# Kernel tuning notes

Hardware: AMD Instinct MI355X
Metric: run time of the kernel (lower is better)

## Reference

```python
import jax, jax.numpy as jnp
import numpy as np

B, T, E, C, H = 8, 96, 96, 256, 8
D = C // H
HID = int(C * 4.0)
EPS = 1e-5


def _ln(x, g, b):
    m = x.mean(-1, keepdims=True)
    v = ((x - m) ** 2).mean(-1, keepdims=True)
    return (x - m) * jax.lax.rsqrt(v + EPS) * g + b


def setup_inputs() -> dict:
    key = jax.random.key(0)
    ks = jax.random.split(key, 20)
    s = 0.02
    inp = {
        "x": jax.random.normal(ks[0], (B, T, E, C), jnp.float32),
        "adj_mask": jax.random.uniform(ks[1], (E, E), jnp.float32) * 2.0 - 1.0,  # direction cosines in [-1,1]
        "n1_g": jnp.ones((C,)), "n1_b": jnp.zeros((C,)),
        "s_wq": jax.random.normal(ks[2], (C, C)) * s,
        "s_wk": jax.random.normal(ks[3], (C, C)) * s,
        "s_wv": jax.random.normal(ks[4], (C, C)) * s,
        "s_wp": jax.random.normal(ks[5], (C, C)) * s,
        "s_bp": jnp.zeros((C,)),
        "s_ng": jnp.ones((C,)), "s_nb": jnp.zeros((C,)),
        "s_gamma": jax.random.normal(ks[6], (1,)) * 0.1,
        "n2_g": jnp.ones((C,)), "n2_b": jnp.zeros((C,)),
        "t_wq": jax.random.normal(ks[7], (C, C)) * s,
        "t_wk": jax.random.normal(ks[8], (C, C)) * s,
        "t_wv": jax.random.normal(ks[9], (C, C)) * s,
        "t_wp": jax.random.normal(ks[10], (C, C)) * s,
        "t_bp": jnp.zeros((C,)),
        "t_gamma": jax.random.normal(ks[11], (1,)) * 0.1,
        "n3_g": jnp.ones((C,)), "n3_b": jnp.zeros((C,)),
        "m_w1": jax.random.normal(ks[12], (C, HID)) * s,
        "m_b1": jnp.zeros((HID,)),
        "m_w2": jax.random.normal(ks[13], (HID, C)) * s,
        "m_b2": jnp.zeros((C,)),
    }
    return inp


def _interp_linear_T(x, t_new):
    # x: [B, T, E, C]; torch F.interpolate(mode='linear', align_corners=False) over T
    t = x.shape[1]
    scale = t / t_new
    src = (jnp.arange(t_new, dtype=jnp.float32) + 0.5) * scale - 0.5
    src = jnp.clip(src, 0.0, t - 1)
    i0 = jnp.floor(src).astype(jnp.int32)
    i1 = jnp.minimum(i0 + 1, t - 1)
    w = (src - i0.astype(jnp.float32))[None, :, None, None]
    return x[:, i0] * (1.0 - w) + x[:, i1] * w


def reference(x, adj_mask, n1_g, n1_b, s_wq, s_wk, s_wv, s_wp, s_bp, s_ng, s_nb, s_gamma,
              n2_g, n2_b, t_wq, t_wk, t_wv, t_wp, t_bp, t_gamma,
              n3_g, n3_b, m_w1, m_b1, m_w2, m_b2):
    b, t, e, c = x.shape
    h, d = H, C // H

    # ---- spatial geometric-cosine attention (per frame) ----
    xs = _ln(x, n1_g, n1_b)                                    # identity inside spatial_attn
    q = (xs @ s_wq).reshape(b, t, e, h, d)
    k = (xs @ s_wk).reshape(b, t, e, h, d)
    v = (xs @ s_wv).reshape(b, t, e, h, d)
    attn = jnp.einsum('btqhd,btkhd->bthqk', q, k)
    attn = (attn * adj_mask + 1.0) * 0.5                        # masked-cosine, no softmax
    o = jnp.einsum('bthqk,btkhd->btqhd', attn, v).reshape(b, t, e, c)
    o = _ln(o @ s_wp + s_bp, s_ng, s_nb)
    x = x + (xs + s_gamma * o)

    # ---- temporal softmax attention (per edge) ----
    xt = _ln(x, n2_g, n2_b)
    q = (xt @ t_wq).reshape(b, t, e, h, d)
    k = (xt @ t_wk).reshape(b, t, e, h, d)
    v = (xt @ t_wv).reshape(b, t, e, h, d)
    attn = jnp.einsum('bqehd,bkehd->behqk', q, k) * (d ** -0.5)
    attn = jax.nn.softmax(attn, axis=-1)
    o = jnp.einsum('behqk,bkehd->bqehd', attn, v).reshape(b, t, e, c)
    o = o @ t_wp + t_bp
    x = x + t_gamma * o

    # ---- MLP ----
    xm = _ln(x, n3_g, n3_b)
    x = x + (jax.nn.gelu(xm @ m_w1 + m_b1, approximate=False) @ m_w2 + m_b2)

    # ---- temporal downsampling (interpolate) ----
    t_new = t // 2 + t % 2
    if t > 1:
        x = _interp_linear_T(x, t_new)
    return x
```

## Files before the change

### kernel.cpp

```cpp
#include <hip/hip_runtime.h>
#include <cmath>

constexpr int BB = 8, TT = 96, EE = 96, CC = 256, HHD = 8, DDm = 32;
constexpr int NTOK = BB * TT * EE;
constexpr int TOUT = TT / 2;

typedef unsigned short u16;
typedef short bf16x8 __attribute__((ext_vector_type(8)));
typedef float f32x4 __attribute__((ext_vector_type(4)));

__device__ __forceinline__ float bf2f(u16 u) {
  union { unsigned int i; float f; } v; v.i = ((unsigned int)u) << 16; return v.f;
}
__device__ __forceinline__ u16 f2bf(float f) {
  union { unsigned int i; float f; } v; v.f = f;
  return (u16)((v.i + 0x7FFFu + ((v.i >> 16) & 1u)) >> 16);
}
__device__ __forceinline__ float wsum(float v) {
#pragma unroll
  for (int off = 32; off; off >>= 1) v += __shfl_xor(v, off);
  return v;
}
__device__ __forceinline__ float gelu_f(float x) {
  return 0.5f * x * (1.0f + erff(x * 0.70710678118654752f));
}
__device__ __forceinline__ int remap_row(int row, int mode) {
  if (mode == 0) return row;
  int b = row / (TT * EE);
  int rem = row - b * (TT * EE);
  if (mode == 1) { int t = rem / EE, e = rem - t * EE; return (b * EE + e) * TT + t; }
  int e = rem / TT, t = rem - e * TT;
  return (b * TT + t) * EE + e;
}

struct WPtr8 { const float* p[8]; };
__global__ void k_transpose8(WPtr8 src, u16* __restrict__ dst) {
  const float* in = src.p[blockIdx.y];
  u16* out = dst + (size_t)blockIdx.y * 65536;
  int idx = blockIdx.x * 256 + threadIdx.x;
  int k = idx >> 8, c = idx & 255;
  out[c * 256 + k] = f2bf(in[idx]);
}

__global__ void k_transpose(const float* __restrict__ in, u16* __restrict__ out, int K, int Nc, int n) {
  int idx = blockIdx.x * 256 + threadIdx.x;
  if (idx < n) {
    int k = idx / Nc, c = idx - k * Nc;
    out[c * K + k] = f2bf(in[idx]);
  }
}

__global__ void k_cvt(const float* __restrict__ in, u16* __restrict__ out, int n) {
  int idx = blockIdx.x * 256 + threadIdx.x;
  if (idx < n) out[idx] = f2bf(in[idx]);
}

__global__ __launch_bounds__(256) void k_ln_in(const float* __restrict__ x,
                                               u16* __restrict__ A, const float* __restrict__ g,
                                               const float* __restrict__ b) {
  int wv = threadIdx.x >> 6, lane = threadIdx.x & 63;
  long tok = (long)blockIdx.x * 4 + wv;
  int c = lane * 4;
  long off = tok * CC + c;
  float4 v = *(const float4*)(x + off);
  float s = v.x + v.y + v.z + v.w;
  float sq = v.x * v.x + v.y * v.y + v.z * v.z + v.w * v.w;
  s = wsum(s); sq = wsum(sq);
  float m = s * (1.0f / CC);
  float rs = rsqrtf(sq * (1.0f / CC) - m * m + 1e-5f);
  float4 gv = *(const float4*)(g + c);
  float4 bv = *(const float4*)(b + c);
  ushort4 o;
  o.x = f2bf((v.x - m) * rs * gv.x + bv.x);
  o.y = f2bf((v.y - m) * rs * gv.y + bv.y);
  o.z = f2bf((v.z - m) * rs * gv.z + bv.z);
  o.w = f2bf((v.w - m) * rs * gv.w + bv.w);
  *(ushort4*)(A + off) = o;
}

__global__ __launch_bounds__(256) void k_ln_f32(const float* __restrict__ X, u16* __restrict__ A,
                                                const float* __restrict__ g, const float* __restrict__ b) {
  int wv = threadIdx.x >> 6, lane = threadIdx.x & 63;
  long tok = (long)blockIdx.x * 4 + wv;
  int c = lane * 4;
  long off = tok * CC + c;
  float4 v = *(const float4*)(X + off);
  float s = v.x + v.y + v.z + v.w;
  float sq = v.x * v.x + v.y * v.y + v.z * v.z + v.w * v.w;
  s = wsum(s); sq = wsum(sq);
  float m = s * (1.0f / CC);
  float rs = rsqrtf(sq * (1.0f / CC) - m * m + 1e-5f);
  float4 gv = *(const float4*)(g + c);
  float4 bv = *(const float4*)(b + c);
  ushort4 o;
  o.x = f2bf((v.x - m) * rs * gv.x + bv.x);
  o.y = f2bf((v.y - m) * rs * gv.y + bv.y);
  o.z = f2bf((v.z - m) * rs * gv.z + bv.z);
  o.w = f2bf((v.w - m) * rs * gv.w + bv.w);
  *(ushort4*)(A + off) = o;
}

__global__ __launch_bounds__(256) void k_sp_combine(const float* __restrict__ xin, float* __restrict__ X,
                                                    u16* __restrict__ A, const u16* __restrict__ P,
                                                    const float* __restrict__ n1g, const float* __restrict__ n1b,
                                                    const float* __restrict__ sg,
                                                    const float* __restrict__ s_ng, const float* __restrict__ s_nb,
                                                    const float* __restrict__ n2g, const float* __restrict__ n2b) {
  int wv = threadIdx.x >> 6, lane = threadIdx.x & 63;
  long tok = (long)blockIdx.x * 4 + wv;
  int c = lane * 4;
  long off = tok * CC + c;
  float4 xv = *(const float4*)(xin + off);
  float s1 = xv.x + xv.y + xv.z + xv.w;
  float q1 = xv.x * xv.x + xv.y * xv.y + xv.z * xv.z + xv.w * xv.w;
  s1 = wsum(s1); q1 = wsum(q1);
  float m1 = s1 * (1.0f / CC);
  float r1 = rsqrtf(q1 * (1.0f / CC) - m1 * m1 + 1e-5f);
  float4 g1 = *(const float4*)(n1g + c);
  float4 b1 = *(const float4*)(n1b + c);
  float xs0 = (xv.x - m1) * r1 * g1.x + b1.x;
  float xs1 = (xv.y - m1) * r1 * g1.y + b1.y;
  float xs2 = (xv.z - m1) * r1 * g1.z + b1.z;
  float xs3 = (xv.w - m1) * r1 * g1.w + b1.w;
  ushort4 up = *(const ushort4*)(P + off);
  float4 p = make_float4(bf2f(up.x), bf2f(up.y), bf2f(up.z), bf2f(up.w));
  float s = p.x + p.y + p.z + p.w;
  float sq = p.x * p.x + p.y * p.y + p.z * p.z + p.w * p.w;
  s = wsum(s); sq = wsum(sq);
  float m = s * (1.0f / CC);
  float rs = rsqrtf(sq * (1.0f / CC) - m * m + 1e-5f);
  float4 ug = *(const float4*)(s_ng + c);
  float4 ub = *(const float4*)(s_nb + c);
  float o0 = (p.x - m) * rs * ug.x + ub.x;
  float o1 = (p.y - m) * rs * ug.y + ub.y;
  float o2 = (p.z - m) * rs * ug.z + ub.z;
  float o3 = (p.w - m) * rs * ug.w + ub.w;
  float gsg = sg[0];
  float x0 = xv.x + xs0 + gsg * o0;
  float x1 = xv.y + xs1 + gsg * o1;
  float x2 = xv.z + xs2 + gsg * o2;
  float x3 = xv.w + xs3 + gsg * o3;
  *(float4*)(X + off) = make_float4(x0, x1, x2, x3);
  float s2 = x0 + x1 + x2 + x3;
  float sq2 = x0 * x0 + x1 * x1 + x2 * x2 + x3 * x3;
  s2 = wsum(s2); sq2 = wsum(sq2);
  float m2 = s2 * (1.0f / CC);
  float rs2 = rsqrtf(sq2 * (1.0f / CC) - m2 * m2 + 1e-5f);
  float4 g2 = *(const float4*)(n2g + c);
  float4 b2 = *(const float4*)(n2b + c);
  ushort4 o;
  o.x = f2bf((x0 - m2) * rs2 * g2.x + b2.x);
  o.y = f2bf((x1 - m2) * rs2 * g2.y + b2.y);
  o.z = f2bf((x2 - m2) * rs2 * g2.z + b2.z);
  o.w = f2bf((x3 - m2) * rs2 * g2.w + b2.w);
  *(ushort4*)(A + off) = o;
}

__global__ __launch_bounds__(256) void k_gemm128(const u16* __restrict__ act, const u16* __restrict__ Wt,
                                                 const float* __restrict__ bias, const float* __restrict__ gptr,
                                                 u16* __restrict__ outB, float* __restrict__ Xacc,
                                                 int Kd, int Nc, int lda, int ldb, int epi, int remap) {
  __shared__ __align__(16) u16 smem[128 * 136];
  u16* As = smem;
  u16* Bs = smem + 4096;
  int m0 = blockIdx.y * 128, n0 = blockIdx.x * 128;
  int tid = threadIdx.x;
  int wv = tid >> 6, lane = tid & 63, lm = lane & 15, quad = lane >> 4;
  int wr = wv >> 1, wc = wv & 1;
  f32x4 acc[4][4];
#pragma unroll
  for (int i = 0; i < 4; i++)
#pragma unroll
    for (int j = 0; j < 4; j++) acc[i][j] = (f32x4){0.f, 0.f, 0.f, 0.f};

  for (int kk = 0; kk < Kd; kk += 32) {
#pragma unroll
    for (int j = 0; j < 2; j++) {
      int cid = j * 256 + wv * 64 + lane;
      int row = cid >> 2, seg = cid & 3;
      const u16* ga = act + (long)(m0 + row) * lda + kk + seg * 8;
      const u16* gb = Wt + (long)(n0 + row) * ldb + kk + seg * 8;
      u16* la = &As[(j * 256 + wv * 64) * 8];
      u16* lb = &Bs[(j * 256 + wv * 64) * 8];
      __builtin_amdgcn_global_load_lds(ga, la, 16, 0, 0);
      __builtin_amdgcn_global_load_lds(gb, lb, 16, 0, 0);
    }
    __syncthreads();
    bf16x8 af[4], bfv[4];
#pragma unroll
    for (int t = 0; t < 4; t++) {
      af[t] = *(const bf16x8*)&As[(wr * 64 + t * 16 + lm) * 32 + quad * 8];
      bfv[t] = *(const bf16x8*)&Bs[(wc * 64 + t * 16 + lm) * 32 + quad * 8];
    }
#pragma unroll
    for (int ti = 0; ti < 4; ti++)
#pragma unroll
      for (int tj = 0; tj < 4; tj++)
        acc[ti][tj] = __builtin_amdgcn_mfma_f32_16x16x32_bf16(af[ti], bfv[tj], acc[ti][tj], 0, 0, 0);
    __syncthreads();
  }

  if (epi == 3) {
    float gm = gptr ? gptr[0] : 1.0f;
#pragma unroll
    for (int tj = 0; tj < 4; tj++) {
      int col = n0 + wc * 64 + tj * 16 + lm;
      float bv = bias ? bias[col] : 0.0f;
#pragma unroll
      for (int ti = 0; ti < 4; ti++)
#pragma unroll
        for (int r = 0; r < 4; r++) {
          int row = remap_row(m0 + wr * 64 + ti * 16 + quad * 4 + r, remap);
          Xacc[(long)row * Nc + col] += gm * (acc[ti][tj][r] + bv);
        }
    }
  } else {
#pragma unroll
    for (int tj = 0; tj < 4; tj++) {
      int col = wc * 64 + tj * 16 + lm;
      float bv = (epi >= 1 && bias) ? bias[n0 + col] : 0.0f;
#pragma unroll
      for (int ti = 0; ti < 4; ti++)
#pragma unroll
        for (int r = 0; r < 4; r++) {
          float vv = acc[ti][tj][r] + bv;
          if (epi == 2) vv = gelu_f(vv);
          smem[(wr * 64 + ti * 16 + quad * 4 + r) * 136 + col] = f2bf(vv);
        }
    }
    __syncthreads();
#pragma unroll
    for (int p = 0; p < 8; p++) {
      int idx = p * 256 + tid;
      int row = idx >> 4, c8 = idx & 15;
      int grow = remap_row(m0 + row, remap);
      *(uint4*)(outB + (long)grow * Nc + n0 + c8 * 8) = *(const uint4*)&smem[row * 136 + c8 * 8];
    }
  }
}

__global__ __launch_bounds__(384) void k_sp_attn(const u16* __restrict__ QKV, const u16* __restrict__ adj,
                                                 u16* __restrict__ O) {
  __shared__ __align__(16) u16 Qs[96 * 32];
  __shared__ __align__(16) u16 Ks[96 * 32];
  __shared__ __align__(16) u16 Vs[96 * 32];
  __shared__ __align__(16) u16 Ss[96 * 96];
  int blk = blockIdx.x;
  int h = blk & 7, t = (blk >> 3) % TT, b = blk / (8 * TT);
  long base = ((long)(b * TT + t) * EE) * 768 + h * DDm;
  int tid = threadIdx.x;
  {
    int row = tid >> 2, seg = tid & 3;
    long goff = base + (long)row * 768 + seg * 8;
    *(uint4*)&Qs[row * 32 + seg * 8] = *(const uint4*)(QKV + goff);
    *(uint4*)&Ks[row * 32 + seg * 8] = *(const uint4*)(QKV + goff + 256);
    *(uint4*)&Vs[row * 32 + seg * 8] = *(const uint4*)(QKV + goff + 512);
#pragma unroll
    for (int i = 0; i < 3; i++) {
      int off = tid * 24 + i * 8;
      *(uint4*)&Ss[off] = *(const uint4*)(adj + off);
    }
  }
  __syncthreads();
  int wv = tid >> 6, lane = tid & 63, lm = lane & 15, quad = lane >> 4;
  bf16x8 aq = *(const bf16x8*)&Qs[(wv * 16 + lm) * 32 + quad * 8];
  f32x4 sc[6];
#pragma unroll
  for (int j = 0; j < 6; j++) {
    bf16x8 bk = *(const bf16x8*)&Ks[(j * 16 + lm) * 32 + quad * 8];
    f32x4 z = (f32x4){0.f, 0.f, 0.f, 0.f};
    sc[j] = __builtin_amdgcn_mfma_f32_16x16x32_bf16(aq, bk, z, 0, 0, 0);
  }
  u16 sv[6][4];
#pragma unroll
  for (int j = 0; j < 6; j++) {
    int col = j * 16 + lm;
#pragma unroll
    for (int r = 0; r < 4; r++) {
      int row = wv * 16 + quad * 4 + r;
      float a = bf2f(Ss[row * 96 + col]);
      sv[j][r] = f2bf((sc[j][r] * a + 1.0f) * 0.5f);
    }
  }
  __syncthreads();
#pragma unroll
  for (int j = 0; j < 6; j++) {
    int col = j * 16 + lm;
#pragma unroll
    for (int r = 0; r < 4; r++) Ss[(wv * 16 + quad * 4 + r) * 96 + col] = sv[j][r];
  }
  __syncthreads();
  f32x4 oc[2];
  oc[0] = (f32x4){0.f, 0.f, 0.f, 0.f};
  oc[1] = (f32x4){0.f, 0.f, 0.f, 0.f};
#pragma unroll
  for (int ks = 0; ks < 3; ks++) {
    bf16x8 as = *(const bf16x8*)&Ss[(wv * 16 + lm) * 96 + ks * 32 + quad * 8];
#pragma unroll
    for (int n = 0; n < 2; n++) {
      bf16x8 bv;
#pragma unroll
      for (int jj = 0; jj < 8; jj++)
        bv[jj] = (short)Vs[(ks * 32 + quad * 8 + jj) * 32 + n * 16 + lm];
      oc[n] = __builtin_amdgcn_mfma_f32_16x16x32_bf16(as, bv, oc[n], 0, 0, 0);
    }
  }
  long obase = ((long)(b * TT + t) * EE) * CC + h * DDm;
#pragma unroll
  for (int n = 0; n < 2; n++)
#pragma unroll
    for (int r = 0; r < 4; r++) {
      int row = wv * 16 + quad * 4 + r;
      O[obase + (long)row * CC + n * 16 + lm] = f2bf(oc[n][r]);
    }
}

__global__ __launch_bounds__(384) void k_tp_attn(const u16* __restrict__ QKV, u16* __restrict__ O) {
  __shared__ __align__(16) u16 Qs[96 * 32];
  __shared__ __align__(16) u16 Ks[96 * 32];
  __shared__ __align__(16) u16 Vs[96 * 32];
  __shared__ __align__(16) u16 Ss[96 * 96];
  int blk = blockIdx.x;
  int h = blk & 7, e = (blk >> 3) % EE, b = blk / (8 * EE);
  long base = ((long)(b * EE + e) * TT) * 768 + h * DDm;
  int tid = threadIdx.x;
  {
    int row = tid >> 2, seg = tid & 3;
    long goff = base + (long)row * 768 + seg * 8;
    *(uint4*)&Qs[row * 32 + seg * 8] = *(const uint4*)(QKV + goff);
    *(uint4*)&Ks[row * 32 + seg * 8] = *(const uint4*)(QKV + goff + 256);
    *(uint4*)&Vs[row * 32 + seg * 8] = *(const uint4*)(QKV + goff + 512);
  }
  __syncthreads();
  int wv = tid >> 6, lane = tid & 63, lm = lane & 15, quad = lane >> 4;
  bf16x8 aq = *(const bf16x8*)&Qs[(wv * 16 + lm) * 32 + quad * 8];
  f32x4 sc[6];
#pragma unroll
  for (int j = 0; j < 6; j++) {
    bf16x8 bk = *(const bf16x8*)&Ks[(j * 16 + lm) * 32 + quad * 8];
    f32x4 z = (f32x4){0.f, 0.f, 0.f, 0.f};
    sc[j] = __builtin_amdgcn_mfma_f32_16x16x32_bf16(aq, bk, z, 0, 0, 0);
  }
  const float scale = 0.17677669529663687f;
#pragma unroll
  for (int r = 0; r < 4; r++) {
    float mx = -1e30f;
#pragma unroll
    for (int j = 0; j < 6; j++) { sc[j][r] *= scale; mx = fmaxf(mx, sc[j][r]); }
#pragma unroll
    for (int mask = 1; mask < 16; mask <<= 1) mx = fmaxf(mx, __shfl_xor(mx, mask));
    float sum = 0.f;
#pragma unroll
    for (int j = 0; j < 6; j++) { float p = __expf(sc[j][r] - mx); sc[j][r] = p; sum += p; }
#pragma unroll
    for (int mask = 1; mask < 16; mask <<= 1) sum += __shfl_xor(sum, mask);
    float inv = 1.0f / sum;
#pragma unroll
    for (int j = 0; j < 6; j++) sc[j][r] *= inv;
  }
#pragma unroll
  for (int j = 0; j < 6; j++) {
    int col = j * 16 + lm;
#pragma unroll
    for (int r = 0; r < 4; r++) Ss[(wv * 16 + quad * 4 + r) * 96 + col] = f2bf(sc[j][r]);
  }
  __syncthreads();
  f32x4 oc[2];
  oc[0] = (f32x4){0.f, 0.f, 0.f, 0.f};
  oc[1] = (f32x4){0.f, 0.f, 0.f, 0.f};
#pragma unroll
  for (int ks = 0; ks < 3; ks++) {
    bf16x8 as = *(const bf16x8*)&Ss[(wv * 16 + lm) * 96 + ks * 32 + quad * 8];
#pragma unroll
    for (int n = 0; n < 2; n++) {
      bf16x8 bv;
#pragma unroll
      for (int jj = 0; jj < 8; jj++)
        bv[jj] = (short)Vs[(ks * 32 + quad * 8 + jj) * 32 + n * 16 + lm];
      oc[n] = __builtin_amdgcn_mfma_f32_16x16x32_bf16(as, bv, oc[n], 0, 0, 0);
    }
  }
  long obase = ((long)(b * EE + e) * TT) * CC + h * DDm;
#pragma unroll
  for (int n = 0; n < 2; n++)
#pragma unroll
    for (int r = 0; r < 4; r++) {
      int row = wv * 16 + quad * 4 + r;
      O[obase + (long)row * CC + n * 16 + lm] = f2bf(oc[n][r]);
    }
}

__global__ __launch_bounds__(256) void k_down(const float* __restrict__ X, float* __restrict__ out) {
  long i4 = ((long)blockIdx.x * 256 + threadIdx.x) * 4;
  long tmp = i4;
  int c = (int)(tmp & 255); tmp >>= 8;
  int e = (int)(tmp % EE); tmp /= EE;
  int i = (int)(tmp % TOUT);
  int b = (int)(tmp / TOUT);
  long src0 = (((long)b * TT + 2 * i) * EE + e) * CC + c;
  float4 a = *(const float4*)(X + src0);
  float4 bb = *(const float4*)(X + src0 + (long)EE * CC);
  float4 o = make_float4(0.5f * (a.x + bb.x), 0.5f * (a.y + bb.y),
                         0.5f * (a.z + bb.z), 0.5f * (a.w + bb.w));
  *(float4*)(out + i4) = o;
}

extern "C" void kernel_launch(void* const* d_in, const int* in_sizes, int n_in,
                              void* d_out, int out_size, void* d_ws, size_t ws_size,
                              hipStream_t stream) {
  (void)in_sizes; (void)n_in; (void)out_size; (void)ws_size;
  const float* x   = (const float*)d_in[0];
  const float* adj = (const float*)d_in[1];
  const float* n1g = (const float*)d_in[2];
  const float* n1b = (const float*)d_in[3];
  const float* swq = (const float*)d_in[4];
  const float* swk = (const float*)d_in[5];
  const float* swv = (const float*)d_in[6];
  const float* swp = (const float*)d_in[7];
  const float* sbp = (const float*)d_in[8];
  const float* sng = (const float*)d_in[9];
  const float* snb = (const float*)d_in[10];
  const float* sg  = (const float*)d_in[11];
  const float* n2g = (const float*)d_in[12];
  const float* n2b = (const float*)d_in[13];
  const float* twq = (const float*)d_in[14];
  const float* twk = (const float*)d_in[15];
  const float* twv = (const float*)d_in[16];
  const float* twp = (const float*)d_in[17];
  const float* tbp = (const float*)d_in[18];
  const float* tg  = (const float*)d_in[19];
  const float* n3g = (const float*)d_in[20];
  const float* n3b = (const float*)d_in[21];
  const float* mw1 = (const float*)d_in[22];
  const float* mb1 = (const float*)d_in[23];
  const float* mw2 = (const float*)d_in[24];
  const float* mb2 = (const float*)d_in[25];
  float* out = (float*)d_out;

  size_t nc = (size_t)NTOK * CC;
  float* X  = (float*)d_ws;
  u16* A    = (u16*)(X + nc);
  u16* QKV  = A + nc;
  u16* Pb   = QKV;
  u16* Hh   = QKV;
  u16* wts  = QKV + 3 * nc;
  u16* swq_t = wts;
  u16* swp_t = wts + 3 * 65536;
  u16* twq_t = wts + 4 * 65536;
  u16* twp_t = wts + 7 * 65536;
  u16* w1_t  = wts + 8 * 65536;
  u16* w2_t  = w1_t + 262144;
  u16* adj_b = w2_t + 262144;

  WPtr8 w8; w8.p[0] = swq; w8.p[1] = swk; w8.p[2] = swv; w8.p[3] = swp;
  w8.p[4] = twq; w8.p[5] = twk; w8.p[6] = twv; w8.p[7] = twp;
  k_transpose8<<<dim3(256, 8), 256, 0, stream>>>(w8, wts);
  k_transpose<<<(256 * 1024 + 255) / 256, 256, 0, stream>>>(mw1, w1_t, 256, 1024, 256 * 1024);
  k_transpose<<<(1024 * 256 + 255) / 256, 256, 0, stream>>>(mw2, w2_t, 1024, 256, 1024 * 256);
  k_cvt<<<(EE * EE + 255) / 256, 256, 0, stream>>>(adj, adj_b, EE * EE);

  auto gemm = [&](const u16* act, const u16* Wt, const float* bias, const float* gamma,
                  u16* outB, float* Xacc, int Kd, int Nc, int lda, int ldb, int epi, int remap, int M) {
    dim3 g(Nc / 128, M / 128);
    k_gemm128<<<g, 256, 0, stream>>>(act, Wt, bias, gamma, outB, Xacc, Kd, Nc, lda, ldb, epi, remap);
  };

  int lnBlocks = NTOK / 4;

  k_ln_in<<<lnBlocks, 256, 0, stream>>>(x, A, n1g, n1b);
  gemm(A, swq_t, nullptr, nullptr, QKV, nullptr, 256, 768, 256, 256, 0, 0, NTOK);
  k_sp_attn<<<BB * TT * HHD, 384, 0, stream>>>(QKV, adj_b, A);
  gemm(A, swp_t, sbp, nullptr, Pb, nullptr, 256, 256, 256, 256, 1, 0, NTOK);
  k_sp_combine<<<lnBlocks, 256, 0, stream>>>(x, X, A, Pb, n1g, n1b, sg, sng, snb, n2g, n2b);

  gemm(A, twq_t, nullptr, nullptr, QKV, nullptr, 256, 768, 256, 256, 0, 1, NTOK);
  k_tp_attn<<<BB * EE * HHD, 384, 0, stream>>>(QKV, A);
  gemm(A, twp_t, tbp, tg, nullptr, X, 256, 256, 256, 256, 3, 2, NTOK);

  k_ln_f32<<<lnBlocks, 256, 0, stream>>>(X, A, n3g, n3b);
  for (int hf = 0; hf < 2; hf++) {
    long r0 = (long)hf * (NTOK / 2);
    gemm(A + r0 * CC, w1_t, mb1, nullptr, Hh, nullptr, 256, 1024, 256, 256, 2, 0, NTOK / 2);
    gemm(Hh, w2_t, mb2, nullptr, nullptr, X + r0 * CC, 1024, 256, 1024, 1024, 3, 0, NTOK / 2);
  }

  long outElems = (long)BB * TOUT * EE * CC;
  k_down<<<(int)(outElems / 4 / 256), 256, 0, stream>>>(X, out);
}
```

Before: 809.3 us.

## Switch to edge-major layout after spatial stage, fuse downsample into MLP GEMM, double-buffer loads

```diff
diff --git a/kernel.cpp b/kernel.cpp
--- a/kernel.cpp
+++ b/kernel.cpp
@@ -23,14 +23,6 @@
 }
 __device__ __forceinline__ float gelu_f(float x) {
   return 0.5f * x * (1.0f + erff(x * 0.70710678118654752f));
-}
-__device__ __forceinline__ int remap_row(int row, int mode) {
-  if (mode == 0) return row;
-  int b = row / (TT * EE);
-  int rem = row - b * (TT * EE);
-  if (mode == 1) { int t = rem / EE, e = rem - t * EE; return (b * EE + e) * TT + t; }
-  int e = rem / TT, t = rem - e * TT;
-  return (b * TT + t) * EE + e;
 }
 
 struct WPtr8 { const float* p[8]; };
@@ -110,6 +102,10 @@
   long tok = (long)blockIdx.x * 4 + wv;
   int c = lane * 4;
   long off = tok * CC + c;
+  int b = (int)(tok / (TT * EE));
+  int rem = (int)(tok - (long)b * TT * EE);
+  int t = rem / EE, e = rem - t * EE;
+  long offB = ((long)(b * EE + e) * TT + t) * CC + c;
   float4 xv = *(const float4*)(xin + off);
   float s1 = xv.x + xv.y + xv.z + xv.w;
   float q1 = xv.x * xv.x + xv.y * xv.y + xv.z * xv.z + xv.w * xv.w;
@@ -140,7 +136,7 @@
   float x1 = xv.y + xs1 + gsg * o1;
   float x2 = xv.z + xs2 + gsg * o2;
   float x3 = xv.w + xs3 + gsg * o3;
-  *(float4*)(X + off) = make_float4(x0, x1, x2, x3);
+  *(float4*)(X + offB) = make_float4(x0, x1, x2, x3);
   float s2 = x0 + x1 + x2 + x3;
   float sq2 = x0 * x0 + x1 * x1 + x2 * x2 + x3 * x3;
   s2 = wsum(s2); sq2 = wsum(sq2);
@@ -153,16 +149,15 @@
   o.y = f2bf((x1 - m2) * rs2 * g2.y + b2.y);
   o.z = f2bf((x2 - m2) * rs2 * g2.z + b2.z);
   o.w = f2bf((x3 - m2) * rs2 * g2.w + b2.w);
-  *(ushort4*)(A + off) = o;
+  *(ushort4*)(A + offB) = o;
 }
 
 __global__ __launch_bounds__(256) void k_gemm128(const u16* __restrict__ act, const u16* __restrict__ Wt,
                                                  const float* __restrict__ bias, const float* __restrict__ gptr,
                                                  u16* __restrict__ outB, float* __restrict__ Xacc,
-                                                 int Kd, int Nc, int lda, int ldb, int epi, int remap) {
-  __shared__ __align__(16) u16 smem[128 * 136];
-  u16* As = smem;
-  u16* Bs = smem + 4096;
+                                                 float* __restrict__ outF,
+                                                 int Kd, int Nc, int lda, int ldb, int epi, int hbase) {
+  __shared__ __align__(16) u16 smem[16384];
   int m0 = blockIdx.y * 128, n0 = blockIdx.x * 128;
   int tid = threadIdx.x;
   int wv = tid >> 6, lane = tid & 63, lm = lane & 15, quad = lane >> 4;
@@ -173,19 +168,28 @@
 #pragma unroll
     for (int j = 0; j < 4; j++) acc[i][j] = (f32x4){0.f, 0.f, 0.f, 0.f};
 
-  for (int kk = 0; kk < Kd; kk += 32) {
+  auto stage = [&](int kt, int buf) {
+    u16* As = smem + buf * 4096;
+    u16* Bs = smem + 8192 + buf * 4096;
 #pragma unroll
     for (int j = 0; j < 2; j++) {
       int cid = j * 256 + wv * 64 + lane;
       int row = cid >> 2, seg = cid & 3;
-      const u16* ga = act + (long)(m0 + row) * lda + kk + seg * 8;
-      const u16* gb = Wt + (long)(n0 + row) * ldb + kk + seg * 8;
-      u16* la = &As[(j * 256 + wv * 64) * 8];
-      u16* lb = &Bs[(j * 256 + wv * 64) * 8];
-      __builtin_amdgcn_global_load_lds(ga, la, 16, 0, 0);
-      __builtin_amdgcn_global_load_lds(gb, lb, 16, 0, 0);
-    }
-    __syncthreads();
+      const u16* ga = act + (long)(m0 + row) * lda + kt * 32 + seg * 8;
+      const u16* gb = Wt + (long)(n0 + row) * ldb + kt * 32 + seg * 8;
+      __builtin_amdgcn_global_load_lds(ga, &As[(j * 256 + wv * 64) * 8], 16, 0, 0);
+      __builtin_amdgcn_global_load_lds(gb, &Bs[(j * 256 + wv * 64) * 8], 16, 0, 0);
+    }
+  };
+
+  int nk = Kd / 32;
+  stage(0, 0);
+  __syncthreads();
+  for (int kt = 0; kt < nk; kt++) {
+    int cur = kt & 1;
+    if (kt + 1 < nk) stage(kt + 1, cur ^ 1);
+    const u16* As = smem + cur * 4096;
+    const u16* Bs = smem + 8192 + cur * 4096;
     bf16x8 af[4], bfv[4];
 #pragma unroll
     for (int t = 0; t < 4; t++) {
@@ -210,31 +214,59 @@
       for (int ti = 0; ti < 4; ti++)
 #pragma unroll
         for (int r = 0; r < 4; r++) {
-          int row = remap_row(m0 + wr * 64 + ti * 16 + quad * 4 + r, remap);
+          int row = m0 + wr * 64 + ti * 16 + quad * 4 + r;
           Xacc[(long)row * Nc + col] += gm * (acc[ti][tj][r] + bv);
         }
     }
+  } else if (epi == 4) {
+#pragma unroll
+    for (int tj = 0; tj < 4; tj++) {
+      int col = n0 + wc * 64 + tj * 16 + lm;
+      float bv = bias ? bias[col] : 0.0f;
+#pragma unroll
+      for (int ti = 0; ti < 4; ti++) {
+        int lr0 = wr * 64 + ti * 16 + quad * 4;
+#pragma unroll
+        for (int pr = 0; pr < 2; pr++) {
+          int lr = lr0 + pr * 2;
+          float v0 = Xacc[(long)(m0 + lr) * Nc + col] + acc[ti][tj][pr * 2] + bv;
+          float v1 = Xacc[(long)(m0 + lr + 1) * Nc + col] + acc[ti][tj][pr * 2 + 1] + bv;
+          int gr = hbase + m0 + lr;
+          int b = gr / (EE * TT);
+          int rem = gr - b * (EE * TT);
+          int e = rem / TT, t = rem - e * TT;
+          long orow = (long)(b * TOUT + (t >> 1)) * EE + e;
+          outF[orow * CC + col] = 0.5f * (v0 + v1);
+        }
+      }
+    }
   } else {
 #pragma unroll
-    for (int tj = 0; tj < 4; tj++) {
-      int col = wc * 64 + tj * 16 + lm;
-      float bv = (epi >= 1 && bias) ? bias[n0 + col] : 0.0f;
-#pragma unroll
-      for (int ti = 0; ti < 4; ti++)
-#pragma unroll
-        for (int r = 0; r < 4; r++) {
-          float vv = acc[ti][tj][r] + bv;
-          if (epi == 2) vv = gelu_f(vv);
-          smem[(wr * 64 + ti * 16 + quad * 4 + r) * 136 + col] = f2bf(vv);
+    for (int h = 0; h < 2; h++) {
+      if (wr == h) {
+#pragma unroll
+        for (int tj = 0; tj < 4; tj++) {
+          int col = wc * 64 + tj * 16 + lm;
+          float bv = (epi >= 1 && bias) ? bias[n0 + col] : 0.0f;
+#pragma unroll
+          for (int ti = 0; ti < 4; ti++)
+#pragma unroll
+            for (int r = 0; r < 4; r++) {
+              float vv = acc[ti][tj][r] + bv;
+              if (epi == 2) vv = gelu_f(vv);
+              smem[(ti * 16 + quad * 4 + r) * 136 + col] = f2bf(vv);
+            }
         }
-    }
-    __syncthreads();
-#pragma unroll
-    for (int p = 0; p < 8; p++) {
-      int idx = p * 256 + tid;
-      int row = idx >> 4, c8 = idx & 15;
-      int grow = remap_row(m0 + row, remap);
-      *(uint4*)(outB + (long)grow * Nc + n0 + c8 * 8) = *(const uint4*)&smem[row * 136 + c8 * 8];
+      }
+      __syncthreads();
+#pragma unroll
+      for (int p = 0; p < 4; p++) {
+        int idx = p * 256 + tid;
+        int row = idx >> 4, c8 = idx & 15;
+        *(uint4*)(outB + (long)(m0 + h * 64 + row) * Nc + n0 + c8 * 8) =
+            *(const uint4*)&smem[row * 136 + c8 * 8];
+      }
+      __syncthreads();
     }
   }
 }
@@ -388,21 +420,6 @@
       int row = wv * 16 + quad * 4 + r;
       O[obase + (long)row * CC + n * 16 + lm] = f2bf(oc[n][r]);
     }
-}
-
-__global__ __launch_bounds__(256) void k_down(const float* __restrict__ X, float* __restrict__ out) {
-  long i4 = ((long)blockIdx.x * 256 + threadIdx.x) * 4;
-  long tmp = i4;
-  int c = (int)(tmp & 255); tmp >>= 8;
-  int e = (int)(tmp % EE); tmp /= EE;
-  int i = (int)(tmp % TOUT);
-  int b = (int)(tmp / TOUT);
-  long src0 = (((long)b * TT + 2 * i) * EE + e) * CC + c;
-  float4 a = *(const float4*)(X + src0);
-  float4 bb = *(const float4*)(X + src0 + (long)EE * CC);
-  float4 o = make_float4(0.5f * (a.x + bb.x), 0.5f * (a.y + bb.y),
-                         0.5f * (a.z + bb.z), 0.5f * (a.w + bb.w));
-  *(float4*)(out + i4) = o;
 }
 
 extern "C" void kernel_launch(void* const* d_in, const int* in_sizes, int n_in,
@@ -460,30 +477,31 @@
   k_cvt<<<(EE * EE + 255) / 256, 256, 0, stream>>>(adj, adj_b, EE * EE);
 
   auto gemm = [&](const u16* act, const u16* Wt, const float* bias, const float* gamma,
-                  u16* outB, float* Xacc, int Kd, int Nc, int lda, int ldb, int epi, int remap, int M) {
+                  u16* outB, float* Xacc, float* outF,
+                  int Kd, int Nc, int lda, int ldb, int epi, int hbase, int M) {
     dim3 g(Nc / 128, M / 128);
-    k_gemm128<<<g, 256, 0, stream>>>(act, Wt, bias, gamma, outB, Xacc, Kd, Nc, lda, ldb, epi, remap);
+    k_gemm128<<<g, 256, 0, stream>>>(act, Wt, bias, gamma, outB, Xacc, outF,
+                                     Kd, Nc, lda, ldb, epi, hbase);
   };
 
   int lnBlocks = NTOK / 4;
 
   k_ln_in<<<lnBlocks, 256, 0, stream>>>(x, A, n1g, n1b);
-  gemm(A, swq_t, nullptr, nullptr, QKV, nullptr, 256, 768, 256, 256, 0, 0, NTOK);
+  gemm(A, swq_t, nullptr, nullptr, QKV, nullptr, nullptr, 256, 768, 256, 256, 0, 0, NTOK);
   k_sp_attn<<<BB * TT * HHD, 384, 0, stream>>>(QKV, adj_b, A);
-  gemm(A, swp_t, sbp, nullptr, Pb, nullptr, 256, 256, 256, 256, 1, 0, NTOK);
+  gemm(A, swp_t, sbp, nullptr, Pb, nullptr, nullptr, 256, 256, 256, 256, 1, 0, NTOK);
   k_sp_combine<<<lnBlocks, 256, 0, stream>>>(x, X, A, Pb, n1g, n1b, sg, sng, snb, n2g, n2b);
 
-  gemm(A, twq_t, nullptr, nullptr, QKV, nullptr, 256, 768, 256, 256, 0, 1, NTOK);
+  gemm(A, twq_t, nullptr, nullptr, QKV, nullptr, nullptr, 256, 768, 256, 256, 0, 0, NTOK);
   k_tp_attn<<<BB * EE * HHD, 384, 0, stream>>>(QKV, A);
-  gemm(A, twp_t, tbp, tg, nullptr, X, 256, 256, 256, 256, 3, 2, NTOK);
+  gemm(A, twp_t, tbp, tg, nullptr, X, nullptr, 256, 256, 256, 256, 3, 0, NTOK);
 
   k_ln_f32<<<lnBlocks, 256, 0, stream>>>(X, A, n3g, n3b);
   for (int hf = 0; hf < 2; hf++) {
-    long r0 = (long)hf * (NTOK / 2);
-    gemm(A + r0 * CC, w1_t, mb1, nullptr, Hh, nullptr, 256, 1024, 256, 256, 2, 0, NTOK / 2);
-    gemm(Hh, w2_t, mb2, nullptr, nullptr, X + r0 * CC, 1024, 256, 1024, 1024, 3, 0, NTOK / 2);
-  }
-
-  long outElems = (long)BB * TOUT * EE * CC;
-  k_down<<<(int)(outElems / 4 / 256), 256, 0, stream>>>(X, out);
-}
+    int hbase = hf * (NTOK / 2);
+    gemm(A + (long)hbase * CC, w1_t, mb1, nullptr, Hh, nullptr, nullptr,
+         256, 1024, 256, 256, 2, 0, NTOK / 2);
+    gemm(Hh, w2_t, mb2, nullptr, nullptr, X + (long)hbase * CC, out,
+         1024, 256, 1024, 1024, 4, hbase, NTOK / 2);
+  }
+}
```

After: 886.4 us. 9.5% more time.
